# Kernel tuning notes

Measured on AMD Instinct MI355X. Metric: run time of the kernel, lower is better.

## Reference

```python
import jax, jax.numpy as jnp
import numpy as np

HID = 1024
NH = 16
DH = HID // NH  # 64


def _heads(x):
    # [B, S, H] -> [B, nH, S, dh]
    B, S, _ = x.shape
    return x.reshape(B, S, NH, DH).transpose(0, 2, 1, 3)


def setup_inputs() -> dict:
    key = jax.random.key(0)
    ks = jax.random.split(key, 16)
    inp = {
        "word_hidden_states": jax.random.normal(ks[0], (2, 2048, HID), jnp.float32),
        "entity_hidden_states": jax.random.normal(ks[1], (2, 256, HID), jnp.float32),
    }
    scale = 1.0 / np.sqrt(HID)
    names = ["Wq", "Wk", "Wv", "Ww2e", "We2w", "We2e"]
    for i, n in enumerate(names):
        inp[n] = jax.random.normal(ks[2 + i], (HID, HID), jnp.float32) * scale
        inp["b" + n[1:]] = jnp.zeros((HID,), jnp.float32)
    return inp


def reference(word_hidden_states, entity_hidden_states,
              Wq, bq, Wk, bk, Wv, bv,
              Ww2e, bw2e, We2w, be2w, We2e, be2e):
    word, ent = word_hidden_states, entity_hidden_states
    B, Sw, _ = word.shape
    Se = ent.shape[1]
    hs = jnp.concatenate([word, ent], axis=1)  # [B, Sw+Se, H]

    # four query types, heads: [B, nH, S*, dh]
    q_w2w = _heads(word @ Wq + bq)
    q_w2e = _heads(word @ Ww2e + bw2e)
    q_e2w = _heads(ent @ We2w + be2w)
    q_e2e = _heads(ent @ We2e + be2e)

    k = _heads(hs @ Wk + bk)
    v = _heads(hs @ Wv + bv)
    k_w, k_e = k[:, :, :Sw, :], k[:, :, Sw:, :]

    # block scores
    s_w2w = jnp.einsum("bhqd,bhkd->bhqk", q_w2w, k_w)  # [B,nH,Sw,Sw]
    s_w2e = jnp.einsum("bhqd,bhkd->bhqk", q_w2e, k_e)  # [B,nH,Sw,Se]
    s_e2w = jnp.einsum("bhqd,bhkd->bhqk", q_e2w, k_w)  # [B,nH,Se,Sw]
    s_e2e = jnp.einsum("bhqd,bhkd->bhqk", q_e2e, k_e)  # [B,nH,Se,Se]

    word_scores = jnp.concatenate([s_w2w, s_w2e], axis=3)
    ent_scores = jnp.concatenate([s_e2w, s_e2e], axis=3)
    scores = jnp.concatenate([word_scores, ent_scores], axis=2)  # [B,nH,S,S]
    scores = scores / np.sqrt(DH)

    probs = jax.nn.softmax(scores, axis=-1)  # dropout is identity in eval
    ctx = jnp.einsum("bhqk,bhkd->bhqd", probs, v)  # [B,nH,S,dh]
    ctx = ctx.transpose(0, 2, 1, 3).reshape(B, Sw + Se, HID)
    return ctx[:, :Sw, :], ctx[:, Sw:, :]
```

## Files before the change

kernel.cpp:

```cpp
#include <hip/hip_runtime.h>
#include <hip/hip_bf16.h>

typedef __attribute__((ext_vector_type(8))) short short8;
typedef __attribute__((ext_vector_type(4))) float f32x4;
typedef __attribute__((ext_vector_type(16))) float f32x16;
typedef __attribute__((ext_vector_type(4))) unsigned short u16x4;
typedef __attribute__((ext_vector_type(8))) unsigned short u16x8;
typedef __attribute__((ext_vector_type(4))) unsigned int u32x4;

__device__ __forceinline__ unsigned short f2b(float f) {
  __hip_bfloat16 h = __float2bfloat16(f);
  return __builtin_bit_cast(unsigned short, h);
}

__device__ __forceinline__ void gload_lds16(const void* g, void* l) {
  __builtin_amdgcn_global_load_lds(
      (const __attribute__((address_space(1))) unsigned int*)g,
      (__attribute__((address_space(3))) unsigned int*)l, 16, 0, 0);
}

__device__ __forceinline__ f32x16 mfma32(short8 a, short8 b, f32x16 c) {
  return __builtin_amdgcn_mfma_f32_32x32x16_bf16(a, b, c, 0, 0, 0);
}

__device__ __forceinline__ unsigned int cvtpk(float a, float b) {
  unsigned int r;
  asm("v_cvt_pk_bf16_f32 %0, %1, %2" : "=v"(r) : "v"(a), "v"(b));
  return r;
}

__global__ __launch_bounds__(256) void cvt_f32_bf16(const float* __restrict__ s,
                                                    unsigned short* __restrict__ d,
                                                    int n8) {
  int i = blockIdx.x * 256 + threadIdx.x;
  if (i >= n8) return;
  const f32x4* sp = (const f32x4*)s;
  f32x4 a = sp[2 * i];
  f32x4 b = sp[2 * i + 1];
  u16x8 o;
  o[0] = f2b(a[0]); o[1] = f2b(a[1]); o[2] = f2b(a[2]); o[3] = f2b(a[3]);
  o[4] = f2b(b[0]); o[5] = f2b(b[1]); o[6] = f2b(b[2]); o[7] = f2b(b[3]);
  ((u16x8*)d)[i] = o;
}

struct WtransParams {
  const float* w[6];
  unsigned short* wt[6];
};

__global__ __launch_bounds__(256) void wtrans(WtransParams p) {
  __shared__ float t[32][33];
  const int z = blockIdx.z;
  const float* W = p.w[z];
  unsigned short* Wt = p.wt[z];
  const int bx = blockIdx.x;
  const int by = blockIdx.y;
  const int tx = threadIdx.x, ty = threadIdx.y;
#pragma unroll
  for (int i = 0; i < 4; ++i)
    t[ty + 8 * i][tx] = W[(by * 32 + ty + 8 * i) * 1024 + bx * 32 + tx];
  __syncthreads();
#pragma unroll
  for (int i = 0; i < 4; ++i)
    Wt[(bx * 32 + ty + 8 * i) * 1024 + by * 32 + tx] = f2b(t[tx][ty + 8 * i]);
}

struct GemmJob {
  const unsigned short* Wt;
  const float* bias;
  unsigned short* out;
  int S;
  int s_off;
  int sshift;
  int trans;
  float scale;
};
struct Gemm2Params {
  const unsigned short* Aw;
  const unsigned short* Ae;
  GemmJob job[8];
};

__global__ __launch_bounds__(256) void gemm_qkv(Gemm2Params p) {
  __shared__ unsigned short As[128 * 64];
  __shared__ unsigned short Bs[128 * 64];
  const int tid = threadIdx.x;
  const int w = tid >> 6, lane = tid & 63;
  const int c = lane & 15, g = lane >> 4;
  const int z = blockIdx.z;
  const int y = blockIdx.y;
  const bool isw = y < 32;
  const GemmJob j = p.job[isw ? z : z + 4];
  const unsigned short* A = isw ? p.Aw : p.Ae;
  const long arow0 = (long)(isw ? y : y - 32) * 128;
  const unsigned short* B = j.Wt;
  const long brow0 = (long)blockIdx.x * 128;

  f32x4 acc[4][4] = {};

  for (int kt = 0; kt < 16; ++kt) {
    __syncthreads();
#pragma unroll
    for (int i = 0; i < 4; ++i) {
      int ch = i * 256 + tid;
      int row = ch >> 3;
      int k8 = ((ch & 7) ^ (row & 7)) << 3;
      const unsigned short* ga = A + (arow0 + row) * 1024 + kt * 64 + k8;
      const unsigned short* gb = B + (brow0 + row) * 1024 + kt * 64 + k8;
      gload_lds16(ga, As + (i * 256 + w * 64) * 8);
      gload_lds16(gb, Bs + (i * 256 + w * 64) * 8);
    }
    __syncthreads();
#pragma unroll
    for (int kf = 0; kf < 2; ++kf) {
      short8 av[4], bv[4];
#pragma unroll
      for (int mf = 0; mf < 4; ++mf) {
        int row = (w >> 1) * 64 + mf * 16 + c;
        int byte = (row * 128 + (kf * 32 + g * 8) * 2) ^ ((row & 7) << 4);
        av[mf] = *(const short8*)((const char*)As + byte);
      }
#pragma unroll
      for (int nf = 0; nf < 4; ++nf) {
        int row = (w & 1) * 64 + nf * 16 + c;
        int byte = (row * 128 + (kf * 32 + g * 8) * 2) ^ ((row & 7) << 4);
        bv[nf] = *(const short8*)((const char*)Bs + byte);
      }
      __builtin_amdgcn_s_setprio(1);
#pragma unroll
      for (int mf = 0; mf < 4; ++mf)
#pragma unroll
        for (int nf = 0; nf < 4; ++nf)
          acc[mf][nf] = __builtin_amdgcn_mfma_f32_16x16x32_bf16(av[mf], bv[nf],
                                                                acc[mf][nf], 0, 0, 0);
      __builtin_amdgcn_s_setprio(0);
    }
  }

  float biasv[4];
#pragma unroll
  for (int nf = 0; nf < 4; ++nf) {
    int n = (int)brow0 + (w & 1) * 64 + nf * 16 + c;
    biasv[nf] = j.bias[n];
  }
  const int smask = (1 << j.sshift) - 1;
  if (j.trans) {
#pragma unroll
    for (int mf = 0; mf < 4; ++mf) {
      int m0 = (int)arow0 + (w >> 1) * 64 + mf * 16 + g * 4;
      int b_ = m0 >> j.sshift;
      int s = (m0 & smask) + j.s_off;
#pragma unroll
      for (int nf = 0; nf < 4; ++nf) {
        int n = (int)brow0 + (w & 1) * 64 + nf * 16 + c;
        int hh = n >> 6, dd = n & 63;
        u16x4 pv;
#pragma unroll
        for (int r = 0; r < 4; ++r)
          pv[r] = f2b((acc[mf][nf][r] + biasv[nf]) * j.scale);
        *(u16x4*)(j.out + (((long)b_ * 16 + hh) * 64 + dd) * 2304 + s) = pv;
      }
    }
  } else {
#pragma unroll
    for (int mf = 0; mf < 4; ++mf) {
#pragma unroll
      for (int r = 0; r < 4; ++r) {
        int m = (int)arow0 + (w >> 1) * 64 + mf * 16 + g * 4 + r;
        int b_ = m >> j.sshift;
        int s = (m & smask) + j.s_off;
#pragma unroll
        for (int nf = 0; nf < 4; ++nf) {
          int n = (int)brow0 + (w & 1) * 64 + nf * 16 + c;
          int hh = n >> 6, dd = n & 63;
          float v = (acc[mf][nf][r] + biasv[nf]) * j.scale;
          j.out[(((long)b_ * 16 + hh) * j.S + s) * 64 + dd] = f2b(v);
        }
      }
    }
  }
}

__global__ __launch_bounds__(256) void attn_kernel(
    const unsigned short* __restrict__ qw2w, const unsigned short* __restrict__ qw2e,
    const unsigned short* __restrict__ qe2w, const unsigned short* __restrict__ qe2e,
    const unsigned short* __restrict__ Kg, const unsigned short* __restrict__ Vtg,
    float* __restrict__ po0, float* __restrict__ po1, float* __restrict__ lbuf) {
  __shared__ unsigned short smem[16384];

  const int tid = threadIdx.x;
  const int w = tid >> 6, lane = tid & 63;
  const int l31 = lane & 31, hf = lane >> 5;

  const int flat = blockIdx.x;
  const int work = (flat & 7) * 144 + (flat >> 3);
  const int part = work & 1;
  const int tile = (work % 36) >> 1;
  const int hb = work / 36;
  const int head = hb & 15, b = hb >> 4;

  const bool isw = tile < 16;
  const int Sq = isw ? 2048 : 256;
  const int q0 = (isw ? tile : tile - 16) * 128 + w * 32;
  const int bh = b * 16 + head;
  const unsigned short* Qa =
      (isw ? qw2w : qe2w) + ((long)bh * Sq + q0 + l31) * 64 + hf * 8;
  const unsigned short* Qb =
      (isw ? qw2e : qe2e) + ((long)bh * Sq + q0 + l31) * 64 + hf * 8;
  const unsigned short* Kb = Kg + (long)bh * 2304 * 64;
  const unsigned short* Vtb = Vtg + (long)bh * 64 * 2304;

  short8 qcur[4];
#pragma unroll
  for (int kf = 0; kf < 4; ++kf) qcur[kf] = *(const short8*)(Qa + kf * 16);

  f32x16 o[2] = {};
  float lrun = 0.f;

  auto stage = [&](int t, int bufi) {
    const unsigned short* Kt = Kb + t * 4096;
    unsigned short* Klp = smem + bufi * 4096;
    unsigned short* Vlp = smem + 8192 + bufi * 4096;
#pragma unroll
    for (int i = 0; i < 2; ++i) {
      int ch = i * 256 + tid;
      int row = ch >> 3, c8 = ch & 7;
      int col = (c8 ^ (row & 7)) << 3;
      gload_lds16(Kt + row * 64 + col, Klp + (i * 256 + (tid & 192)) * 8);
      gload_lds16(Vtb + row * 2304 + t * 64 + col, Vlp + (i * 256 + (tid & 192)) * 8);
    }
  };

  const int t0 = part * 18, t1 = t0 + 18;
  stage(t0, 0);
  __syncthreads();
  int cur = 0;

  for (int t = t0; t < t1; ++t) {
    if (t == 32) {
#pragma unroll
      for (int kf = 0; kf < 4; ++kf) qcur[kf] = *(const short8*)(Qb + kf * 16);
    }
    if (t + 1 < t1) stage(t + 1, cur ^ 1);

    const char* Kbase = (const char*)(smem + cur * 4096);
    const char* Vbase = (const char*)(smem + 8192 + cur * 4096);

    f32x16 st[2] = {};
#pragma unroll
    for (int kg = 0; kg < 2; ++kg) {
      int row = kg * 32 + l31;
      int rb = (row * 128) | (hf * 16);
      int sw = (row & 7) << 4;
      short8 kfr[4];
#pragma unroll
      for (int kf = 0; kf < 4; ++kf)
        kfr[kf] = *(const short8*)(Kbase + ((rb + kf * 32) ^ sw));
      __builtin_amdgcn_s_setprio(1);
#pragma unroll
      for (int kf = 0; kf < 4; ++kf) st[kg] = mfma32(kfr[kf], qcur[kf], st[kg]);
      __builtin_amdgcn_s_setprio(0);
    }

    float s0 = 0.f, s1 = 0.f, s2 = 0.f, s3 = 0.f;
#pragma unroll
    for (int kg = 0; kg < 2; ++kg) {
#pragma unroll
      for (int r = 0; r < 16; r += 4) {
        float p0 = __builtin_amdgcn_exp2f(st[kg][r + 0]);
        float p1 = __builtin_amdgcn_exp2f(st[kg][r + 1]);
        float p2 = __builtin_amdgcn_exp2f(st[kg][r + 2]);
        float p3 = __builtin_amdgcn_exp2f(st[kg][r + 3]);
        st[kg][r + 0] = p0; st[kg][r + 1] = p1;
        st[kg][r + 2] = p2; st[kg][r + 3] = p3;
        s0 += p0; s1 += p1; s2 += p2; s3 += p3;
      }
    }
    lrun += (s0 + s1) + (s2 + s3);

#pragma unroll
    for (int kg = 0; kg < 2; ++kg)
#pragma unroll
      for (int hs = 0; hs < 2; ++hs) {
        const int rbase = hs * 8;
        unsigned int a0 = cvtpk(st[kg][rbase + 0], st[kg][rbase + 1]);
        unsigned int a1 = cvtpk(st[kg][rbase + 2], st[kg][rbase + 3]);
        unsigned int b0 = cvtpk(st[kg][rbase + 4], st[kg][rbase + 5]);
        unsigned int b1 = cvtpk(st[kg][rbase + 6], st[kg][rbase + 7]);
        asm("v_permlane32_swap_b32 %0, %1" : "+v"(a0), "+v"(b0));
        asm("v_permlane32_swap_b32 %0, %1" : "+v"(a1), "+v"(b1));
        u32x4 pw;
        pw[0] = a0; pw[1] = a1; pw[2] = b0; pw[3] = b1;
        short8 pf = __builtin_bit_cast(short8, pw);
        const int ks = kg * 2 + hs;
        short8 vf0, vf1;
        {
          int row = l31;
          int byte = ((row * 128) | (ks * 32 + hf * 16)) ^ ((row & 7) << 4);
          vf0 = *(const short8*)(Vbase + byte);
          row = 32 + l31;
          byte = ((row * 128) | (ks * 32 + hf * 16)) ^ ((row & 7) << 4);
          vf1 = *(const short8*)(Vbase + byte);
        }
        __builtin_amdgcn_s_setprio(1);
        o[0] = mfma32(vf0, pf, o[0]);
        o[1] = mfma32(vf1, pf, o[1]);
        __builtin_amdgcn_s_setprio(0);
      }

    __syncthreads();
    cur ^= 1;
  }

  float ltot = lrun + __shfl_xor(lrun, 32);

  const int sgb = (isw ? 0 : 2048) + q0;
  if (hf == 0) lbuf[(long)part * 73728 + bh * 2304 + sgb + l31] = ltot;

  float* E = (float*)smem + w * 2048;
#pragma unroll
  for (int mf = 0; mf < 2; ++mf)
#pragma unroll
    for (int rg = 0; rg < 4; ++rg) {
      int d0 = mf * 32 + rg * 8 + hf * 4;
      f32x4 v;
      v[0] = o[mf][rg * 4 + 0];
      v[1] = o[mf][rg * 4 + 1];
      v[2] = o[mf][rg * 4 + 2];
      v[3] = o[mf][rg * 4 + 3];
      *(f32x4*)(E + l31 * 64 + (d0 ^ ((l31 & 7) << 2))) = v;
    }

  float* po = part ? po1 : po0;
  float* ob = isw ? po + (((long)b * 2048 + q0) * 1024 + head * 64)
                  : po + (long)2 * 2048 * 1024 +
                        (((long)b * 256 + q0) * 1024 + head * 64);
#pragma unroll
  for (int i = 0; i < 8; ++i) {
    int qr = (lane >> 4) + i * 4;
    int dc = (lane & 15) * 4;
    f32x4 v = *(const f32x4*)(E + qr * 64 + (dc ^ ((qr & 7) << 2)));
    *(f32x4*)(ob + (long)qr * 1024 + dc) = v;
  }
}

__global__ __launch_bounds__(256) void attn_merge(const float* __restrict__ po0,
                                                  const float* __restrict__ po1,
                                                  const float* __restrict__ lbuf,
                                                  float* __restrict__ out) {
  long i = ((long)blockIdx.x * 256 + threadIdx.x) * 4;
  if (i >= 4718592) return;
  int bh, sg;
  if (i < 4194304) {
    int b = (int)(i >> 21), s = (int)((i >> 10) & 2047), h = (int)((i >> 6) & 15);
    bh = b * 16 + h;
    sg = s;
  } else {
    long j = i - 4194304;
    int b = (int)(j >> 18), s = (int)((j >> 10) & 255), h = (int)((j >> 6) & 15);
    bh = b * 16 + h;
    sg = 2048 + s;
  }
  float l0 = lbuf[bh * 2304 + sg];
  float l1 = lbuf[73728 + bh * 2304 + sg];
  f32x4 a = *(const f32x4*)(po0 + i);
  f32x4 c = *(const f32x4*)(po1 + i);
  float inv = 1.f / (l0 + l1);
  f32x4 r = (a + c) * inv;
  *(f32x4*)(out + i) = r;
}

extern "C" void kernel_launch(void* const* d_in, const int* in_sizes, int n_in,
                              void* d_out, int out_size, void* d_ws, size_t ws_size,
                              hipStream_t stream) {
  (void)in_sizes; (void)n_in; (void)out_size; (void)ws_size;
  const float* word = (const float*)d_in[0];
  const float* ent = (const float*)d_in[1];

  char* ws = (char*)d_ws;
  size_t off = 0;
  auto alloc = [&](size_t bytes) {
    void* p = ws + off;
    off += (bytes + 255) & ~(size_t)255;
    return p;
  };
  unsigned short* Xw = (unsigned short*)alloc(4096ull * 1024 * 2);
  unsigned short* Xe = (unsigned short*)alloc(512ull * 1024 * 2);
  unsigned short* Wt[6];
  for (int i = 0; i < 6; ++i) Wt[i] = (unsigned short*)alloc(1024ull * 1024 * 2);
  unsigned short* qw2w = (unsigned short*)alloc(2ull * 16 * 2048 * 64 * 2);
  unsigned short* qw2e = (unsigned short*)alloc(2ull * 16 * 2048 * 64 * 2);
  unsigned short* qe2w = (unsigned short*)alloc(2ull * 16 * 256 * 64 * 2);
  unsigned short* qe2e = (unsigned short*)alloc(2ull * 16 * 256 * 64 * 2);
  unsigned short* Kbuf = (unsigned short*)alloc(2ull * 16 * 2304 * 64 * 2);
  unsigned short* Vtbuf = (unsigned short*)alloc(2ull * 16 * 64 * 2304 * 2);
  float* po1 = (float*)alloc(4718592ull * 4);
  float* lbuf = (float*)alloc(2ull * 73728 * 4);
  float* po0 = (float*)ws;

  cvt_f32_bf16<<<2048, 256, 0, stream>>>(word, Xw, 524288);
  cvt_f32_bf16<<<256, 256, 0, stream>>>(ent, Xe, 65536);

  WtransParams wp;
  wp.w[0] = (const float*)d_in[2];
  wp.w[1] = (const float*)d_in[4];
  wp.w[2] = (const float*)d_in[6];
  wp.w[3] = (const float*)d_in[8];
  wp.w[4] = (const float*)d_in[10];
  wp.w[5] = (const float*)d_in[12];
  for (int i = 0; i < 6; ++i) wp.wt[i] = Wt[i];
  wtrans<<<dim3(32, 32, 6), dim3(32, 8), 0, stream>>>(wp);

  const float* bq = (const float*)d_in[3];
  const float* bk = (const float*)d_in[5];
  const float* bv = (const float*)d_in[7];
  const float* bw2e = (const float*)d_in[9];
  const float* be2w = (const float*)d_in[11];
  const float* be2e = (const float*)d_in[13];
  const float qs = 0.125f * 1.44269504f;

  Gemm2Params gp;
  gp.Aw = Xw;
  gp.Ae = Xe;
  gp.job[0] = {Wt[0], bq, qw2w, 2048, 0, 11, 0, qs};
  gp.job[1] = {Wt[3], bw2e, qw2e, 2048, 0, 11, 0, qs};
  gp.job[2] = {Wt[1], bk, Kbuf, 2304, 0, 11, 0, 1.f};
  gp.job[3] = {Wt[2], bv, Vtbuf, 2304, 0, 11, 1, 1.f};
  gp.job[4] = {Wt[4], be2w, qe2w, 256, 0, 8, 0, qs};
  gp.job[5] = {Wt[5], be2e, qe2e, 256, 0, 8, 0, qs};
  gp.job[6] = {Wt[1], bk, Kbuf, 2304, 2048, 8, 0, 1.f};
  gp.job[7] = {Wt[2], bv, Vtbuf, 2304, 2048, 8, 1, 1.f};
  gemm_qkv<<<dim3(8, 36, 4), 256, 0, stream>>>(gp);

  attn_kernel<<<1152, 256, 0, stream>>>(qw2w, qw2e, qe2w, qe2e, Kbuf, Vtbuf,
                                        po0, po1, lbuf);
  attn_merge<<<4608, 256, 0, stream>>>(po0, po1, lbuf, (float*)d_out);
}
```

Measured before the change: 154.6 us.

## Load V fragments directly from global into registers, halve LDS footprint

V tiles are no longer staged through LDS. Each lane now loads its transposed-V MFMA fragments straight from global memory at the start of every KV tile, so LDS holds only double-buffered K. The epilogue transpose through LDS is split into two 32-column passes, so the shared buffer shrinks from 32KB to 16KB, which could allow more blocks per CU. The tradeoff is that V loads are now uncached 16-byte-per-lane global reads sitting on the critical path before the PV MFMAs, with no prefetch overlap, which adds latency and more global traffic.

```diff
diff --git a/kernel.cpp b/kernel.cpp
--- a/kernel.cpp
+++ b/kernel.cpp
@@ -186,7 +186,7 @@
     const unsigned short* __restrict__ qe2w, const unsigned short* __restrict__ qe2e,
     const unsigned short* __restrict__ Kg, const unsigned short* __restrict__ Vtg,
     float* __restrict__ po0, float* __restrict__ po1, float* __restrict__ lbuf) {
-  __shared__ unsigned short smem[16384];
+  __shared__ unsigned short smem[8192];
 
   const int tid = threadIdx.x;
   const int w = tid >> 6, lane = tid & 63;
@@ -220,14 +220,12 @@
   auto stage = [&](int t, int bufi) {
     const unsigned short* Kt = Kb + t * 4096;
     unsigned short* Klp = smem + bufi * 4096;
-    unsigned short* Vlp = smem + 8192 + bufi * 4096;
 #pragma unroll
     for (int i = 0; i < 2; ++i) {
       int ch = i * 256 + tid;
       int row = ch >> 3, c8 = ch & 7;
       int col = (c8 ^ (row & 7)) << 3;
       gload_lds16(Kt + row * 64 + col, Klp + (i * 256 + (tid & 192)) * 8);
-      gload_lds16(Vtb + row * 2304 + t * 64 + col, Vlp + (i * 256 + (tid & 192)) * 8);
     }
   };
 
@@ -243,8 +241,15 @@
     }
     if (t + 1 < t1) stage(t + 1, cur ^ 1);
 
+    short8 vfr[4][2];
+#pragma unroll
+    for (int ks = 0; ks < 4; ++ks)
+#pragma unroll
+      for (int mf = 0; mf < 2; ++mf)
+        vfr[ks][mf] = *(const short8*)(Vtb + (mf * 32 + l31) * 2304 + t * 64 +
+                                       ks * 16 + hf * 8);
+
     const char* Kbase = (const char*)(smem + cur * 4096);
-    const char* Vbase = (const char*)(smem + 8192 + cur * 4096);
 
     f32x16 st[2] = {};
 #pragma unroll
@@ -293,18 +298,9 @@
         pw[0] = a0; pw[1] = a1; pw[2] = b0; pw[3] = b1;
         short8 pf = __builtin_bit_cast(short8, pw);
         const int ks = kg * 2 + hs;
-        short8 vf0, vf1;
-        {
-          int row = l31;
-          int byte = ((row * 128) | (ks * 32 + hf * 16)) ^ ((row & 7) << 4);
-          vf0 = *(const short8*)(Vbase + byte);
-          row = 32 + l31;
-          byte = ((row * 128) | (ks * 32 + hf * 16)) ^ ((row & 7) << 4);
-          vf1 = *(const short8*)(Vbase + byte);
-        }
         __builtin_amdgcn_s_setprio(1);
-        o[0] = mfma32(vf0, pf, o[0]);
-        o[1] = mfma32(vf1, pf, o[1]);
+        o[0] = mfma32(vfr[ks][0], pf, o[0]);
+        o[1] = mfma32(vfr[ks][1], pf, o[1]);
         __builtin_amdgcn_s_setprio(0);
       }
 
@@ -316,31 +312,36 @@
 
   const int sgb = (isw ? 0 : 2048) + q0;
   if (hf == 0) lbuf[(long)part * 73728 + bh * 2304 + sgb + l31] = ltot;
-
-  float* E = (float*)smem + w * 2048;
-#pragma unroll
-  for (int mf = 0; mf < 2; ++mf)
-#pragma unroll
-    for (int rg = 0; rg < 4; ++rg) {
-      int d0 = mf * 32 + rg * 8 + hf * 4;
-      f32x4 v;
-      v[0] = o[mf][rg * 4 + 0];
-      v[1] = o[mf][rg * 4 + 1];
-      v[2] = o[mf][rg * 4 + 2];
-      v[3] = o[mf][rg * 4 + 3];
-      *(f32x4*)(E + l31 * 64 + (d0 ^ ((l31 & 7) << 2))) = v;
-    }
 
   float* po = part ? po1 : po0;
   float* ob = isw ? po + (((long)b * 2048 + q0) * 1024 + head * 64)
                   : po + (long)2 * 2048 * 1024 +
                         (((long)b * 256 + q0) * 1024 + head * 64);
-#pragma unroll
-  for (int i = 0; i < 8; ++i) {
-    int qr = (lane >> 4) + i * 4;
-    int dc = (lane & 15) * 4;
-    f32x4 v = *(const f32x4*)(E + qr * 64 + (dc ^ ((qr & 7) << 2)));
-    *(f32x4*)(ob + (long)qr * 1024 + dc) = v;
+
+  float* E = (float*)smem + w * 1024;
+#pragma unroll
+  for (int p = 0; p < 2; ++p) {
+#pragma unroll
+    for (int rg = 0; rg < 4; ++rg) {
+      int off = rg * 8 + hf * 4;
+      f32x4 v;
+      v[0] = o[p][rg * 4 + 0];
+      v[1] = o[p][rg * 4 + 1];
+      v[2] = o[p][rg * 4 + 2];
+      v[3] = o[p][rg * 4 + 3];
+      *(f32x4*)(E + l31 * 32 + (off ^ ((l31 & 7) << 2))) = v;
+    }
+    asm volatile("s_waitcnt lgkmcnt(0)" ::: "memory");
+    __builtin_amdgcn_sched_barrier(0);
+#pragma unroll
+    for (int i = 0; i < 4; ++i) {
+      int qr = i * 8 + (lane >> 3);
+      int cc = (lane & 7) * 4;
+      f32x4 v = *(const f32x4*)(E + qr * 32 + (cc ^ ((qr & 7) << 2)));
+      *(f32x4*)(ob + (long)qr * 1024 + p * 32 + cc) = v;
+    }
+    asm volatile("s_waitcnt lgkmcnt(0)" ::: "memory");
+    __builtin_amdgcn_sched_barrier(0);
   }
 }
 
```

After: 201.8 us. +30.5%, slower.
